# Optimization experiments

Measured on AMD Instinct MI355X. Metric: run time of the kernel, lower is better.

Reference implementation:

```python
import jax, jax.numpy as jnp
import numpy as np

IN_F, T_IN, T_OUT = 8, 96, 32
B = 4096


def _lstm(x, Wih, Whh, b):
    """Standard LSTM (torch gate order i,f,g,o), batch_first. x: [B,T,I] -> [B,T,H].
    Variational dropout with p=0 (eval mode) is identity, so omitted."""
    Bsz = x.shape[0]
    H = Whh.shape[1]
    # precompute input contribution for all timesteps: [B,T,4H]
    xg = jnp.einsum('bti,gi->btg', x, Wih) + b

    def step(carry, xt):
        h, c = carry
        g = xt + h @ Whh.T  # [B,4H]
        i, f, gg, o = jnp.split(g, 4, axis=-1)
        c = jax.nn.sigmoid(f) * c + jax.nn.sigmoid(i) * jnp.tanh(gg)
        h = jax.nn.sigmoid(o) * jnp.tanh(c)
        return (h, c), h

    h0 = jnp.zeros((Bsz, H), x.dtype)
    _, ys = jax.lax.scan(step, (h0, h0), jnp.swapaxes(xg, 0, 1))
    return jnp.swapaxes(ys, 0, 1)


def setup_inputs() -> dict:
    key = jax.random.key(0)
    ks = jax.random.split(key, 16)
    s = 0.1  # init scale
    return {
        'x': jax.random.normal(ks[0], (B, T_IN, IN_F), jnp.float32),
        'e1_Wih': s * jax.random.normal(ks[1], (256, IN_F), jnp.float32),
        'e1_Whh': s * jax.random.normal(ks[2], (256, 64), jnp.float32),
        'e1_b': s * jax.random.normal(ks[3], (256,), jnp.float32),
        'e2_Wih': s * jax.random.normal(ks[4], (4, 64), jnp.float32),
        'e2_Whh': s * jax.random.normal(ks[5], (4, 1), jnp.float32),
        'e2_b': s * jax.random.normal(ks[6], (4,), jnp.float32),
        'd1_Wih': s * jax.random.normal(ks[7], (64, 1), jnp.float32),
        'd1_Whh': s * jax.random.normal(ks[8], (64, 16), jnp.float32),
        'd1_b': s * jax.random.normal(ks[9], (64,), jnp.float32),
        'd2_Wih': s * jax.random.normal(ks[10], (4, 16), jnp.float32),
        'd2_Whh': s * jax.random.normal(ks[11], (4, 1), jnp.float32),
        'd2_b': s * jax.random.normal(ks[12], (4,), jnp.float32),
        'fc1_W': s * jax.random.normal(ks[13], (32, T_IN + T_OUT), jnp.float32),
        'fc1_b': s * jax.random.normal(ks[13], (32,), jnp.float32),
        'fc2_W': s * jax.random.normal(ks[14], (T_OUT, 32), jnp.float32),
        'fc2_b': s * jax.random.normal(ks[15], (T_OUT,), jnp.float32),
    }


def reference(x, e1_Wih, e1_Whh, e1_b, e2_Wih, e2_Whh, e2_b,
              d1_Wih, d1_Whh, d1_b, d2_Wih, d2_Whh, d2_b,
              fc1_W, fc1_b, fc2_W, fc2_b):
    # Encoder: LSTM(in->64) -> LSTM(64->1) -> ReLU
    h = _lstm(x, e1_Wih, e1_Whh, e1_b)
    h = _lstm(h, e2_Wih, e2_Whh, e2_b)
    enc_out = jax.nn.relu(h)  # [B, T_IN, 1]
    # Auxiliary: last T_OUT steps of invocation column (col 0)
    x_aux = x[:, -T_OUT:, 0:1]  # [B, T_OUT, 1]
    dec_in = jnp.concatenate([enc_out, x_aux], axis=1)  # [B, T_IN+T_OUT, 1]
    # Decoder: LSTM(1->16) -> LSTM(16->1)
    d = _lstm(dec_in, d1_Wih, d1_Whh, d1_b)
    d = _lstm(d, d2_Wih, d2_Whh, d2_b)  # [B, T_IN+T_OUT, 1]
    # FC head over the flattened time dim
    flat = d.reshape(-1, T_IN + T_OUT)
    out = flat @ fc1_W.T + fc1_b
    out = out @ fc2_W.T + fc2_b
    return out  # [B, T_OUT]
```

## Files before the change

kernel.cpp:

```cpp
#include <hip/hip_runtime.h>
#include <hip/hip_bf16.h>

typedef __attribute__((ext_vector_type(8))) short bf16x8;
typedef __attribute__((ext_vector_type(4))) float f32x4;

__device__ __forceinline__ float sigm(float x) {
    return __builtin_amdgcn_rcpf(1.0f + __expf(-x));
}
__device__ __forceinline__ float tanh_(float x) {
    float e = __expf(2.0f * x);
    return 1.0f - 2.0f * __builtin_amdgcn_rcpf(e + 1.0f);
}
__device__ __forceinline__ ushort f2bf(float f) {
    uint u = __float_as_uint(f);
    u = u + 0x7FFFu + ((u >> 16) & 1u);
    return (ushort)(u >> 16);
}
__device__ __forceinline__ float bf2f(ushort s) { return __uint_as_float(((uint)s) << 16); }

__global__ __launch_bounds__(1024) __attribute__((amdgpu_waves_per_eu(4, 4)))
void k1_enc(
    const float* __restrict__ x,
    const float* __restrict__ e1_Wih, const float* __restrict__ e1_Whh, const float* __restrict__ e1_b,
    const float* __restrict__ e2_Wih, const float* __restrict__ e2_b,
    const float* __restrict__ e2_Whh,
    float* __restrict__ dec_in)
{
    __shared__ float x_s[16 * 772];
    __shared__ __align__(16) ushort h_hi[2][8][16][8];
    __shared__ __align__(16) ushort h_lo[2][8][16][8];
    __shared__ __align__(16) ushort x2_s[2][4][16][8];
    __shared__ __align__(16) float pe2_s[96 * 64];

    const int t = threadIdx.x;
    const int bBase = blockIdx.x * 16;
    const int wv = t >> 6, l = t & 63;
    const int row = l & 15, sub = l >> 4;

    for (int bb = 0; bb < 16; ++bb)
        for (int i = t; i < 768; i += 1024)
            x_s[bb * 772 + i] = x[(size_t)(bBase + bb) * 768 + i];

    auto loadW = [&](const float* rowbase, int k0, bool valid, bf16x8& hi8, bf16x8& lo8) {
        float f[8];
        if (valid) {
            float4 v0 = ((const float4*)(rowbase + k0))[0];
            float4 v1 = ((const float4*)(rowbase + k0))[1];
            f[0]=v0.x; f[1]=v0.y; f[2]=v0.z; f[3]=v0.w;
            f[4]=v1.x; f[5]=v1.y; f[6]=v1.z; f[7]=v1.w;
        } else {
            #pragma unroll
            for (int j = 0; j < 8; ++j) f[j] = 0.f;
        }
        #pragma unroll
        for (int j = 0; j < 8; ++j) {
            ushort h = f2bf(f[j]);
            hi8[j] = (short)h;
            lo8[j] = (short)f2bf(f[j] - bf2f(h));
        }
    };
    auto loadA = [&](int T, bool isE2, bf16x8& Ah0, bf16x8& Ah1, bf16x8& Al0, bf16x8& Al1, bf16x8& A2) {
        const int gate = row & 3, uq = row >> 2;
        const bool valid = !isE2 || (uq == 0);
        const int wr = isE2 ? gate : gate * 64 + T * 4 + uq;
        const float* rp = isE2 ? (e2_Wih + (size_t)wr * 64) : (e1_Whh + (size_t)wr * 64);
        loadW(rp, sub * 8,      valid, Ah0, Al0);
        loadW(rp, 32 + sub * 8, valid, Ah1, Al1);
        #pragma unroll
        for (int j = 0; j < 8; ++j) A2[j] = 0;
        if (valid) {
            if (!isE2) {
                if (sub < 3) {
                    const float* wihr = e1_Wih + (size_t)wr * 8;
                    #pragma unroll
                    for (int j = 0; j < 8; ++j) {
                        float f = wihr[j];
                        ushort hh = f2bf(f);
                        A2[j] = (sub < 2) ? (short)hh : (short)f2bf(f - bf2f(hh));
                    }
                } else {
                    float bb = e1_b[wr];
                    ushort hh = f2bf(bb);
                    A2[0] = (short)hh; A2[1] = (short)f2bf(bb - bf2f(hh));
                }
            } else if (sub == 3) {
// ... 75 lines not shown
            h_lo[pn][u0_ >> 3][cb][u0_ & 7] = f2bf(hv - bf2f(hh));
        }

        if (ts < 95 && t < 384) {
            int sb = t >> 7, b = (t >> 3) & 15, j = t & 7;
            float xv = x_s[b * 772 + (ts + 1) * 8 + j];
            ushort hi = f2bf(xv);
            x2_s[pn][sb][b][j] = (sb == 1) ? f2bf(xv - bf2f(hi)) : hi;
        }
        __syncthreads();
    }

    if (wv == 15) {
        bf16x8 Bh0 = *(const bf16x8*)&h_hi[0][sub][cb][0];
        bf16x8 Bh1 = *(const bf16x8*)&h_hi[0][4 + sub][cb][0];
        bf16x8 Bl0 = *(const bf16x8*)&h_lo[0][sub][cb][0];
        bf16x8 Bl1 = *(const bf16x8*)&h_lo[0][4 + sub][cb][0];
        bf16x8 Bx  = *(const bf16x8*)&x2_s[0][sub][cb][0];
        f32x4 u2 = {0.f,0.f,0.f,0.f}, v2 = {0.f,0.f,0.f,0.f};
        u2 = __builtin_amdgcn_mfma_f32_16x16x32_bf16(A2h0, Bh0, u2, 0, 0, 0);
        u2 = __builtin_amdgcn_mfma_f32_16x16x32_bf16(A2l0, Bh0, u2, 0, 0, 0);
        u2 = __builtin_amdgcn_mfma_f32_16x16x32_bf16(A2h0, Bl0, u2, 0, 0, 0);
        v2 = __builtin_amdgcn_mfma_f32_16x16x32_bf16(A2h1, Bh1, v2, 0, 0, 0);
        v2 = __builtin_amdgcn_mfma_f32_16x16x32_bf16(A2l1, Bh1, v2, 0, 0, 0);
        v2 = __builtin_amdgcn_mfma_f32_16x16x32_bf16(A2h1, Bl1, v2, 0, 0, 0);
        v2 = __builtin_amdgcn_mfma_f32_16x16x32_bf16(A2x,  Bx,  v2, 0, 0, 0);
        if (sub == 0) {
            f32x4 acc2 = u2 + v2;
            #pragma unroll
            for (int i = 0; i < 4; ++i)
                pe2_s[95 * 64 + i * 16 + cb] = acc2[i];
        }
    }
    __syncthreads();

    if (wv == 0 && l < 16) {
        const float w0 = e2_Whh[0], w1 = e2_Whh[1], w2 = e2_Whh[2], w3 = e2_Whh[3];
        float ni = pe2_s[l], nf = pe2_s[16 + l], ng = pe2_s[32 + l], no = pe2_s[48 + l];
        float h = 0.f, c = 0.f;
        #pragma unroll 1
        for (int ts = 0; ts < 96; ++ts) {
            float gi = ni, gf = nf, gg2 = ng, go = no;
            if (ts < 95) {
                int b2 = (ts + 1) * 64;
                ni = pe2_s[b2 + l]; nf = pe2_s[b2 + 16 + l];
                ng = pe2_s[b2 + 32 + l]; no = pe2_s[b2 + 48 + l];
            }
            gi = fmaf(h, w0, gi);
            gf = fmaf(h, w1, gf);
            gg2 = fmaf(h, w2, gg2);
            go = fmaf(h, w3, go);
            c = fmaf(sigm(gf), c, sigm(gi) * tanh_(gg2));
            h = sigm(go) * tanh_(c);
            dec_in[(size_t)ts * 4096 + bBase + l] = fmaxf(h, 0.f);
        }
    }
    if (wv >= 1 && wv <= 8) {
        int i = (wv - 1) * 64 + l;
        int B = i >> 5, j = i & 31;
        dec_in[(size_t)(96 + j) * 4096 + bBase + B] = x_s[B * 772 + (64 + j) * 8];
    }
}

__global__ __launch_bounds__(256, 2) void k3_dec(
    const float* __restrict__ dec_in,
    const float* __restrict__ d1_Wih, const float* __restrict__ d1_Whh, const float* __restrict__ d1_b,
    const float* __restrict__ d2_Wih, const float* __restrict__ d2_b,
    const float* __restrict__ d2_Whh,
    const float* __restrict__ fc1_W, const float* __restrict__ fc1_b,
    const float* __restrict__ fc2_W, const float* __restrict__ fc2_b,
    float* __restrict__ out)
{
    __shared__ float din_s[16 * 129];
    __shared__ float h_lds[16][16];
    __shared__ float pd2_s[16 * 516];
    __shared__ float d2h_s[16 * 132];
    __shared__ float mid_s[16 * 36];

    const int t = threadIdx.x;
    const int w = t >> 6, lane = t & 63;
    const int qq4 = lane >> 4, u = lane & 15;
    const int row = w * 4 + qq4;
    const size_t bBase = (size_t)blockIdx.x * 16;

    for (int i = t; i < 2048; i += 256) {
        int ts = i >> 4, rr = i & 15;
        din_s[rr * 129 + ts] = dec_in[(size_t)ts * 4096 + bBase + rr];
    }

    float wih_g[4], bg[4], whh_g[4][16], d2w[16];
    #pragma unroll
    for (int g = 0; g < 4; ++g) {
        wih_g[g] = d1_Wih[g * 16 + u];
        bg[g]    = d1_b[g * 16 + u];
        const float4* wp = (const float4*)(d1_Whh + (size_t)(g * 16 + u) * 16);
        #pragma unroll
        for (int k4 = 0; k4 < 4; ++k4) {
            float4 v = wp[k4];
            whh_g[g][4*k4+0] = v.x; whh_g[g][4*k4+1] = v.y;
            whh_g[g][4*k4+2] = v.z; whh_g[g][4*k4+3] = v.w;
        }
    }
    {
        const float4* wp = (const float4*)(d2_Wih + (size_t)(u & 3) * 16);
        #pragma unroll
        for (int k4 = 0; k4 < 4; ++k4) {
            float4 v = wp[k4];
            d2w[4*k4+0] = v.x; d2w[4*k4+1] = v.y; d2w[4*k4+2] = v.z; d2w[4*k4+3] = v.w;
        }
    }
    const float d2bias = d2_b[u & 3];

    float h = 0.f, c = 0.f;
    __syncthreads();

    float hv[16];
    for (int ts = 0; ts < 128; ++ts) {
        float xv = din_s[row * 129 + ts];
        float p0 = fmaf(xv, wih_g[0], bg[0]);
        float p1 = fmaf(xv, wih_g[1], bg[1]);
        float p2 = fmaf(xv, wih_g[2], bg[2]);
        float p3 = fmaf(xv, wih_g[3], bg[3]);
        if (ts > 0) {
            const float4* hp = (const float4*)&h_lds[row][0];
            #pragma unroll
            for (int k4 = 0; k4 < 4; ++k4) {
                float4 v = hp[k4];
                hv[4*k4+0] = v.x; hv[4*k4+1] = v.y; hv[4*k4+2] = v.z; hv[4*k4+3] = v.w;
            }
            #pragma unroll
            for (int k = 0; k < 16; ++k) {
                p0 = fmaf(hv[k], whh_g[0][k], p0);
                p1 = fmaf(hv[k], whh_g[1][k], p1);
                p2 = fmaf(hv[k], whh_g[2][k], p2);
                p3 = fmaf(hv[k], whh_g[3][k], p3);
            }
            if (u < 4) {
                float a = d2bias;
                #pragma unroll
                for (int k = 0; k < 16; ++k) a = fmaf(hv[k], d2w[k], a);
                pd2_s[row * 516 + (ts - 1) * 4 + u] = a;
            }
        }
        c = fmaf(sigm(p1), c, sigm(p0) * tanh_(p2));
        h = sigm(p3) * tanh_(c);
        h_lds[row][u] = h;
    }
    {
        const float4* hp = (const float4*)&h_lds[row][0];
        #pragma unroll
        for (int k4 = 0; k4 < 4; ++k4) {
            float4 v = hp[k4];
            hv[4*k4+0] = v.x; hv[4*k4+1] = v.y; hv[4*k4+2] = v.z; hv[4*k4+3] = v.w;
        }
        if (u < 4) {
            float a = d2bias;
            #pragma unroll
            for (int k = 0; k < 16; ++k) a = fmaf(hv[k], d2w[k], a);
            pd2_s[row * 516 + 127 * 4 + u] = a;
        }
    }
    __syncthreads();

    {
        const float w0 = d2_Whh[0], w1 = d2_Whh[1], w2 = d2_Whh[2], w3 = d2_Whh[3];
        if (t < 16) {
            float4 dbuf[4];
            #pragma unroll
            for (int j = 0; j < 4; ++j) dbuf[j] = *(const float4*)&pd2_s[t * 516 + j * 4];
            float h2 = 0.f, c2 = 0.f;
            #pragma unroll
            for (int ts = 0; ts < 128; ++ts) {
                float4 g4 = dbuf[ts & 3];
                if (ts + 4 < 128) dbuf[ts & 3] = *(const float4*)&pd2_s[t * 516 + (ts + 4) * 4];
                float gi = fmaf(h2, w0, g4.x);
                float gf = fmaf(h2, w1, g4.y);
                float gg = fmaf(h2, w2, g4.z);
                float go = fmaf(h2, w3, g4.w);
                c2 = fmaf(sigm(gf), c2, sigm(gi) * tanh_(gg));
                h2 = sigm(go) * tanh_(c2);
                d2h_s[t * 132 + ts] = h2;
            }
        }
    }
    __syncthreads();

    {
        const int bb = t >> 4, o = t & 15;
        float acc0 = fc1_b[o], acc1 = fc1_b[o + 16];
        const float4* wa = (const float4*)(fc1_W + (size_t)o * 128);
        const float4* wb = (const float4*)(fc1_W + (size_t)(o + 16) * 128);
        const float4* fp = (const float4*)&d2h_s[bb * 132];
        #pragma unroll
        for (int k4 = 0; k4 < 32; ++k4) {
            float4 f = fp[k4], va = wa[k4], vb = wb[k4];
            acc0 = fmaf(f.x, va.x, acc0); acc0 = fmaf(f.y, va.y, acc0);
            acc0 = fmaf(f.z, va.z, acc0); acc0 = fmaf(f.w, va.w, acc0);
            acc1 = fmaf(f.x, vb.x, acc1); acc1 = fmaf(f.y, vb.y, acc1);
            acc1 = fmaf(f.z, vb.z, acc1); acc1 = fmaf(f.w, vb.w, acc1);
        }
        mid_s[bb * 36 + o] = acc0;
        mid_s[bb * 36 + o + 16] = acc1;
        __syncthreads();
        float o0 = fc2_b[o], o1 = fc2_b[o + 16];
        const float4* va2 = (const float4*)(fc2_W + (size_t)o * 32);
        const float4* vb2 = (const float4*)(fc2_W + (size_t)(o + 16) * 32);
        const float4* mp = (const float4*)&mid_s[bb * 36];
        #pragma unroll
        for (int k4 = 0; k4 < 8; ++k4) {
            float4 m = mp[k4], va = va2[k4], vb = vb2[k4];
            o0 = fmaf(m.x, va.x, o0); o0 = fmaf(m.y, va.y, o0);
            o0 = fmaf(m.z, va.z, o0); o0 = fmaf(m.w, va.w, o0);
            o1 = fmaf(m.x, vb.x, o1); o1 = fmaf(m.y, vb.y, o1);
            o1 = fmaf(m.z, vb.z, o1); o1 = fmaf(m.w, vb.w, o1);
        }
        out[(bBase + bb) * 32 + o] = o0;
        out[(bBase + bb) * 32 + o + 16] = o1;
    }
}

extern "C" void kernel_launch(void* const* d_in, const int* in_sizes, int n_in,
                              void* d_out, int out_size, void* d_ws, size_t ws_size,
                              hipStream_t stream) {
    const float* x      = (const float*)d_in[0];
    const float* e1_Wih = (const float*)d_in[1];
    const float* e1_Whh = (const float*)d_in[2];
    const float* e1_b   = (const float*)d_in[3];
    const float* e2_Wih = (const float*)d_in[4];
    const float* e2_Whh = (const float*)d_in[5];
    const float* e2_b   = (const float*)d_in[6];
    const float* d1_Wih = (const float*)d_in[7];
    const float* d1_Whh = (const float*)d_in[8];
    const float* d1_b   = (const float*)d_in[9];
    const float* d2_Wih = (const float*)d_in[10];
    const float* d2_Whh = (const float*)d_in[11];
    const float* d2_b   = (const float*)d_in[12];
    const float* fc1_W  = (const float*)d_in[13];
    const float* fc1_b  = (const float*)d_in[14];
    const float* fc2_W  = (const float*)d_in[15];
    const float* fc2_b  = (const float*)d_in[16];
    float* out = (float*)d_out;

    float* dec_in = (float*)d_ws;

    hipLaunchKernelGGL(k1_enc, dim3(256), dim3(1024), 0, stream,
                       x, e1_Wih, e1_Whh, e1_b, e2_Wih, e2_b, e2_Whh, dec_in);
    hipLaunchKernelGGL(k3_dec, dim3(256), dim3(256), 0, stream,
                       dec_in, d1_Wih, d1_Whh, d1_b, d2_Wih, d2_b, d2_Whh,
                       fc1_W, fc1_b, fc2_W, fc2_b, out);
}
```

Before: 157.3 us.

## Move decoder LSTM recurrence onto bf16 MFMA with split hi/lo precision

```diff
diff --git a/kernel.cpp b/kernel.cpp
--- a/kernel.cpp
+++ b/kernel.cpp
@@ -222,7 +222,8 @@
     }
 }
 
-__global__ __launch_bounds__(256, 2) void k3_dec(
+__global__ __launch_bounds__(512) __attribute__((amdgpu_waves_per_eu(2, 2)))
+void k3_dec(
     const float* __restrict__ dec_in,
     const float* __restrict__ d1_Wih, const float* __restrict__ d1_Whh, const float* __restrict__ d1_b,
     const float* __restrict__ d2_Wih, const float* __restrict__ d2_b,
@@ -231,151 +232,183 @@
     const float* __restrict__ fc2_W, const float* __restrict__ fc2_b,
     float* __restrict__ out)
 {
-    __shared__ float din_s[16 * 129];
-    __shared__ float h_lds[16][16];
-    __shared__ float pd2_s[16 * 516];
-    __shared__ float d2h_s[16 * 132];
-    __shared__ float mid_s[16 * 36];
+    __shared__ float din_s[16][132];
+    __shared__ __align__(16) ushort h_s[8][2][32];
+    __shared__ __align__(16) float pd2_s[8][2][128][4];
+    __shared__ float d2h_s[8][2][128];
+    __shared__ float mid_s[8][2][32];
 
     const int t = threadIdx.x;
-    const int w = t >> 6, lane = t & 63;
-    const int qq4 = lane >> 4, u = lane & 15;
-    const int row = w * 4 + qq4;
+    const int wb = t >> 6, l = t & 63;
+    const int cb = l & 15, sub = l >> 4;
     const size_t bBase = (size_t)blockIdx.x * 16;
 
-    for (int i = t; i < 2048; i += 256) {
-        int ts = i >> 4, rr = i & 15;
-        din_s[rr * 129 + ts] = dec_in[(size_t)ts * 4096 + bBase + rr];
-    }
-
-    float wih_g[4], bg[4], whh_g[4][16], d2w[16];
+    for (int i = t; i < 2048; i += 512) {
+        int ts = i >> 4, bb = i & 15;
+        din_s[bb][ts] = dec_in[(size_t)ts * 4096 + bBase + bb];
+    }
+
+    bf16x8 A1t[5], A2t[5];
+    {
+        const int r = l & 15, g = r & 3, ul = r >> 2;
+        #pragma unroll
+        for (int T = 0; T < 4; ++T) {
+            const int grow = g * 16 + 4 * ul + T;
+            const float* wr = d1_Whh + grow * 16;
+            float wih = d1_Wih[grow], bb = d1_b[grow];
+            ushort wih_hi = f2bf(wih), wih_lo = f2bf(wih - bf2f(wih_hi));
+            ushort b_hi = f2bf(bb),  b_lo  = f2bf(bb - bf2f(b_hi));
+            bf16x8 a1, a2;
+            #pragma unroll
+            for (int j = 0; j < 8; ++j) {
+                int k = sub * 8 + j;
+                float w = wr[k & 15];
+                ushort whi = f2bf(w);
+                a1[j] = (short)whi;
+                if (k < 16) a2[j] = (short)f2bf(w - bf2f(whi));
+                else {
+                    int kk = k - 16;
+                    ushort v = (kk == 0) ? wih_hi : (kk == 1) ? wih_hi :
+                               (kk == 2) ? b_hi   : (kk == 3) ? b_lo   :
+                               (kk == 4) ? wih_lo : (ushort)0;
+                    a2[j] = (short)v;
+                }
+            }
+            A1t[T] = a1; A2t[T] = a2;
+        }
+        {
+            const bool valid = r < 4;
+            const float* wr = d2_Wih + (size_t)(r & 3) * 16;
+            float bb2 = valid ? d2_b[r & 3] : 0.f;
+            ushort b_hi = f2bf(bb2), b_lo = f2bf(bb2 - bf2f(b_hi));
+            bf16x8 a1, a2;
+            #pragma unroll
+            for (int j = 0; j < 8; ++j) {
+                int k = sub * 8 + j;
+                float w = valid ? wr[k & 15] : 0.f;
+                ushort whi = f2bf(w);
+                a1[j] = (short)whi;
+                if (k < 16) a2[j] = (short)f2bf(w - bf2f(whi));
+                else {
+                    int kk = k - 16;
+                    ushort v = (kk == 2) ? b_hi : (kk == 3) ? b_lo : (ushort)0;
+                    a2[j] = valid ? (short)v : (short)0;
+                }
+            }
+            A1t[4] = a1; A2t[4] = a2;
+        }
+    }
+
+    if (l < 64) h_s[wb][l >> 5][l & 31] = 0;
+
+    bf16x8 zero8;
     #pragma unroll
-    for (int g = 0; g < 4; ++g) {
-        wih_g[g] = d1_Wih[g * 16 + u];
-        bg[g]    = d1_b[g * 16 + u];
-        const float4* wp = (const float4*)(d1_Whh + (size_t)(g * 16 + u) * 16);
-        #pragma unroll
-        for (int k4 = 0; k4 < 4; ++k4) {
-            float4 v = wp[k4];
-            whh_g[g][4*k4+0] = v.x; whh_g[g][4*k4+1] = v.y;
-            whh_g[g][4*k4+2] = v.z; whh_g[g][4*k4+3] = v.w;
-        }
-    }
+    for (int j = 0; j < 8; ++j) zero8[j] = 0;
+
+    float c_st[4] = {0.f, 0.f, 0.f, 0.f};
+    const int drow = 2 * wb + (cb & 1);
+    __syncthreads();
+
+    #pragma unroll 1
+    for (int ts = 0; ts < 128; ++ts) {
+        bf16x8 B1 = *(const bf16x8*)&h_s[wb][cb & 1][sub * 8];
+        float xv = din_s[drow][ts];
+        ushort xhi = f2bf(xv), xlo = f2bf(xv - bf2f(xhi));
+        bf16x8 xb = zero8;
+        xb[0] = (short)xhi; xb[1] = (short)xlo;
+        xb[2] = (short)0x3F80; xb[3] = (short)0x3F80; xb[4] = (short)xhi;
+        bf16x8 B2 = (sub < 2) ? B1 : (sub == 2) ? xb : zero8;
+
+        f32x4 z = {0.f, 0.f, 0.f, 0.f};
+        f32x4 a0 = __builtin_amdgcn_mfma_f32_16x16x32_bf16(A1t[0], B1, z, 0, 0, 0);
+        a0 = __builtin_amdgcn_mfma_f32_16x16x32_bf16(A2t[0], B2, a0, 0, 0, 0);
+        f32x4 a1 = __builtin_amdgcn_mfma_f32_16x16x32_bf16(A1t[1], B1, z, 0, 0, 0);
+        a1 = __builtin_amdgcn_mfma_f32_16x16x32_bf16(A2t[1], B2, a1, 0, 0, 0);
+        f32x4 a2 = __builtin_amdgcn_mfma_f32_16x16x32_bf16(A1t[2], B1, z, 0, 0, 0);
+        a2 = __builtin_amdgcn_mfma_f32_16x16x32_bf16(A2t[2], B2, a2, 0, 0, 0);
+        f32x4 a3 = __builtin_amdgcn_mfma_f32_16x16x32_bf16(A1t[3], B1, z, 0, 0, 0);
+        a3 = __builtin_amdgcn_mfma_f32_16x16x32_bf16(A2t[3], B2, a3, 0, 0, 0);
+        f32x4 a4 = __builtin_amdgcn_mfma_f32_16x16x32_bf16(A1t[4], B1, z, 0, 0, 0);
+        a4 = __builtin_amdgcn_mfma_f32_16x16x32_bf16(A2t[4], B2, a4, 0, 0, 0);
+
+        if (ts > 0 && sub == 0 && cb < 2)
+            *(float4*)&pd2_s[wb][cb][ts - 1][0] = make_float4(a4[0], a4[1], a4[2], a4[3]);
+
+        float hn[4];
+        {
+            c_st[0] = fmaf(sigm(a0[1]), c_st[0], sigm(a0[0]) * tanh_(a0[2]));
+            hn[0] = sigm(a0[3]) * tanh_(c_st[0]);
+            c_st[1] = fmaf(sigm(a1[1]), c_st[1], sigm(a1[0]) * tanh_(a1[2]));
+            hn[1] = sigm(a1[3]) * tanh_(c_st[1]);
+            c_st[2] = fmaf(sigm(a2[1]), c_st[2], sigm(a2[0]) * tanh_(a2[2]));
+            hn[2] = sigm(a2[3]) * tanh_(c_st[2]);
+            c_st[3] = fmaf(sigm(a3[1]), c_st[3], sigm(a3[0]) * tanh_(a3[2]));
+            hn[3] = sigm(a3[3]) * tanh_(c_st[3]);
+        }
+        if (cb < 2) {
+            uint2 phi, plo;
+            phi.x = (uint)f2bf(hn[0]) | ((uint)f2bf(hn[1]) << 16);
+            phi.y = (uint)f2bf(hn[2]) | ((uint)f2bf(hn[3]) << 16);
+            plo.x = (uint)f2bf(hn[0] - bf2f(f2bf(hn[0]))) | ((uint)f2bf(hn[1] - bf2f(f2bf(hn[1]))) << 16);
+            plo.y = (uint)f2bf(hn[2] - bf2f(f2bf(hn[2]))) | ((uint)f2bf(hn[3] - bf2f(f2bf(hn[3]))) << 16);
+            *(uint2*)&h_s[wb][cb][4 * sub] = phi;
+            *(uint2*)&h_s[wb][cb][16 + 4 * sub] = plo;
+        }
+    }
+
     {
-        const float4* wp = (const float4*)(d2_Wih + (size_t)(u & 3) * 16);
-        #pragma unroll
-        for (int k4 = 0; k4 < 4; ++k4) {
-            float4 v = wp[k4];
-            d2w[4*k4+0] = v.x; d2w[4*k4+1] = v.y; d2w[4*k4+2] = v.z; d2w[4*k4+3] = v.w;
-        }
-    }
-    const float d2bias = d2_b[u & 3];
-
-    float h = 0.f, c = 0.f;
-    __syncthreads();
-
-    float hv[16];
-    for (int ts = 0; ts < 128; ++ts) {
-        float xv = din_s[row * 129 + ts];
-        float p0 = fmaf(xv, wih_g[0], bg[0]);
-        float p1 = fmaf(xv, wih_g[1], bg[1]);
-        float p2 = fmaf(xv, wih_g[2], bg[2]);
-        float p3 = fmaf(xv, wih_g[3], bg[3]);
-        if (ts > 0) {
-            const float4* hp = (const float4*)&h_lds[row][0];
-            #pragma unroll
-            for (int k4 = 0; k4 < 4; ++k4) {
-                float4 v = hp[k4];
-                hv[4*k4+0] = v.x; hv[4*k4+1] = v.y; hv[4*k4+2] = v.z; hv[4*k4+3] = v.w;
-            }
-            #pragma unroll
-            for (int k = 0; k < 16; ++k) {
-                p0 = fmaf(hv[k], whh_g[0][k], p0);
-                p1 = fmaf(hv[k], whh_g[1][k], p1);
-                p2 = fmaf(hv[k], whh_g[2][k], p2);
-                p3 = fmaf(hv[k], whh_g[3][k], p3);
-            }
-            if (u < 4) {
-                float a = d2bias;
-                #pragma unroll
-                for (int k = 0; k < 16; ++k) a = fmaf(hv[k], d2w[k], a);
-                pd2_s[row * 516 + (ts - 1) * 4 + u] = a;
-            }
-        }
-        c = fmaf(sigm(p1), c, sigm(p0) * tanh_(p2));
-        h = sigm(p3) * tanh_(c);
-        h_lds[row][u] = h;
-    }
+        bf16x8 B1f = *(const bf16x8*)&h_s[wb][cb & 1][sub * 8];
+        bf16x8 onev = zero8; onev[2] = (short)0x3F80; onev[3] = (short)0x3F80;
+        bf16x8 B2f = (sub < 2) ? B1f : (sub == 2) ? onev : zero8;
+        f32x4 z = {0.f, 0.f, 0.f, 0.f};
+        f32x4 a4 = __builtin_amdgcn_mfma_f32_16x16x32_bf16(A1t[4], B1f, z, 0, 0, 0);
+        a4 = __builtin_amdgcn_mfma_f32_16x16x32_bf16(A2t[4], B2f, a4, 0, 0, 0);
+        if (sub == 0 && cb < 2)
+            *(float4*)&pd2_s[wb][cb][127][0] = make_float4(a4[0], a4[1], a4[2], a4[3]);
+    }
+
+    if (l < 2) {
+        const float w0 = d2_Whh[0], w1 = d2_Whh[1], w2 = d2_Whh[2], w3 = d2_Whh[3];
+        float4 dbuf[4];
+        #pragma unroll
+        for (int j = 0; j < 4; ++j) dbuf[j] = *(const float4*)&pd2_s[wb][l][j][0];
+        float h2 = 0.f, c2 = 0.f;
+        #pragma unroll
+        for (int ts = 0; ts < 128; ++ts) {
+            float4 g4 = dbuf[ts & 3];
+            if (ts + 4 < 128) dbuf[ts & 3] = *(const float4*)&pd2_s[wb][l][ts + 4][0];
+            float gi = fmaf(h2, w0, g4.x);
+            float gf = fmaf(h2, w1, g4.y);
+            float gg = fmaf(h2, w2, g4.z);
+            float go = fmaf(h2, w3, g4.w);
+            c2 = fmaf(sigm(gf), c2, sigm(gi) * tanh_(gg));
+            h2 = sigm(go) * tanh_(c2);
+            d2h_s[wb][l][ts] = h2;
+        }
+    }
+
     {
-        const float4* hp = (const float4*)&h_lds[row][0];
-        #pragma unroll
-        for (int k4 = 0; k4 < 4; ++k4) {
-            float4 v = hp[k4];
-            hv[4*k4+0] = v.x; hv[4*k4+1] = v.y; hv[4*k4+2] = v.z; hv[4*k4+3] = v.w;
-        }
-        if (u < 4) {
-            float a = d2bias;
-            #pragma unroll
-            for (int k = 0; k < 16; ++k) a = fmaf(hv[k], d2w[k], a);
-            pd2_s[row * 516 + 127 * 4 + u] = a;
-        }
-    }
-    __syncthreads();
-
-    {
-        const float w0 = d2_Whh[0], w1 = d2_Whh[1], w2 = d2_Whh[2], w3 = d2_Whh[3];
-        if (t < 16) {
-            float4 dbuf[4];
-            #pragma unroll
-            for (int j = 0; j < 4; ++j) dbuf[j] = *(const float4*)&pd2_s[t * 516 + j * 4];
-            float h2 = 0.f, c2 = 0.f;
-            #pragma unroll
-            for (int ts = 0; ts < 128; ++ts) {
-                float4 g4 = dbuf[ts & 3];
-                if (ts + 4 < 128) dbuf[ts & 3] = *(const float4*)&pd2_s[t * 516 + (ts + 4) * 4];
-                float gi = fmaf(h2, w0, g4.x);
-                float gf = fmaf(h2, w1, g4.y);
-                float gg = fmaf(h2, w2, g4.z);
-                float go = fmaf(h2, w3, g4.w);
-                c2 = fmaf(sigm(gf), c2, sigm(gi) * tanh_(gg));
-                h2 = sigm(go) * tanh_(c2);
-                d2h_s[t * 132 + ts] = h2;
-            }
-        }
-    }
-    __syncthreads();
-
-    {
-        const int bb = t >> 4, o = t & 15;
-        float acc0 = fc1_b[o], acc1 = fc1_b[o + 16];
-        const float4* wa = (const float4*)(fc1_W + (size_t)o * 128);
-        const float4* wb = (const float4*)(fc1_W + (size_t)(o + 16) * 128);
-        const float4* fp = (const float4*)&d2h_s[bb * 132];
+        const int cbb = l >> 5, o = l & 31;
+        float acc = fc1_b[o];
+        const float4* wp = (const float4*)(fc1_W + (size_t)o * 128);
+        const float4* fp = (const float4*)&d2h_s[wb][cbb][0];
         #pragma unroll
         for (int k4 = 0; k4 < 32; ++k4) {
-            float4 f = fp[k4], va = wa[k4], vb = wb[k4];
-            acc0 = fmaf(f.x, va.x, acc0); acc0 = fmaf(f.y, va.y, acc0);
-            acc0 = fmaf(f.z, va.z, acc0); acc0 = fmaf(f.w, va.w, acc0);
-            acc1 = fmaf(f.x, vb.x, acc1); acc1 = fmaf(f.y, vb.y, acc1);
-            acc1 = fmaf(f.z, vb.z, acc1); acc1 = fmaf(f.w, vb.w, acc1);
-        }
-        mid_s[bb * 36 + o] = acc0;
-        mid_s[bb * 36 + o + 16] = acc1;
-        __syncthreads();
-        float o0 = fc2_b[o], o1 = fc2_b[o + 16];
-        const float4* va2 = (const float4*)(fc2_W + (size_t)o * 32);
-        const float4* vb2 = (const float4*)(fc2_W + (size_t)(o + 16) * 32);
-        const float4* mp = (const float4*)&mid_s[bb * 36];
+            float4 f = fp[k4], vv = wp[k4];
+            acc = fmaf(f.x, vv.x, acc); acc = fmaf(f.y, vv.y, acc);
+            acc = fmaf(f.z, vv.z, acc); acc = fmaf(f.w, vv.w, acc);
+        }
+        mid_s[wb][cbb][o] = acc;
+        float o2 = fc2_b[o];
+        const float4* w2p = (const float4*)(fc2_W + (size_t)o * 32);
+        const float4* mp = (const float4*)&mid_s[wb][cbb][0];
         #pragma unroll
         for (int k4 = 0; k4 < 8; ++k4) {
-            float4 m = mp[k4], va = va2[k4], vb = vb2[k4];
-            o0 = fmaf(m.x, va.x, o0); o0 = fmaf(m.y, va.y, o0);
-            o0 = fmaf(m.z, va.z, o0); o0 = fmaf(m.w, va.w, o0);
-            o1 = fmaf(m.x, vb.x, o1); o1 = fmaf(m.y, vb.y, o1);
-            o1 = fmaf(m.z, vb.z, o1); o1 = fmaf(m.w, vb.w, o1);
-        }
-        out[(bBase + bb) * 32 + o] = o0;
-        out[(bBase + bb) * 32 + o + 16] = o1;
+            float4 m = mp[k4], vv = w2p[k4];
+            o2 = fmaf(m.x, vv.x, o2); o2 = fmaf(m.y, vv.y, o2);
+            o2 = fmaf(m.z, vv.z, o2); o2 = fmaf(m.w, vv.w, o2);
+        }
+        out[(bBase + 2 * wb + cbb) * 32 + o] = o2;
     }
 }
 
@@ -405,7 +438,7 @@
 
     hipLaunchKernelGGL(k1_enc, dim3(256), dim3(1024), 0, stream,
                        x, e1_Wih, e1_Whh, e1_b, e2_Wih, e2_b, e2_Whh, dec_in);
-    hipLaunchKernelGGL(k3_dec, dim3(256), dim3(256), 0, stream,
+    hipLaunchKernelGGL(k3_dec, dim3(256), dim3(512), 0, stream,
                        dec_in, d1_Wih, d1_Whh, d1_b, d2_Wih, d2_b, d2_Whh,
                        fc1_W, fc1_b, fc2_W, fc2_b, out);
 }
```

New measurement: 240.3 us. 1.53x slower.

## Split decoder LSTM hidden dot across lane pairs and keep each row in one wave

Applied to the files above, without the earlier changes.

```diff
diff --git a/kernel.cpp b/kernel.cpp
--- a/kernel.cpp
+++ b/kernel.cpp
@@ -222,7 +222,8 @@
     }
 }
 
-__global__ __launch_bounds__(256, 2) void k3_dec(
+__global__ __launch_bounds__(512) __attribute__((amdgpu_waves_per_eu(2, 2)))
+void k3_dec(
     const float* __restrict__ dec_in,
     const float* __restrict__ d1_Wih, const float* __restrict__ d1_Whh, const float* __restrict__ d1_b,
     const float* __restrict__ d2_Wih, const float* __restrict__ d2_b,
@@ -231,36 +232,34 @@
     const float* __restrict__ fc2_W, const float* __restrict__ fc2_b,
     float* __restrict__ out)
 {
-    __shared__ float din_s[16 * 129];
-    __shared__ float h_lds[16][16];
-    __shared__ float pd2_s[16 * 516];
-    __shared__ float d2h_s[16 * 132];
-    __shared__ float mid_s[16 * 36];
+    __shared__ float din_s[16][132];
+    __shared__ __align__(16) float h_f[16][20];
+    __shared__ __align__(16) float pd2_s[16][130][4];
+    __shared__ float d2h_s[16][132];
+    __shared__ float mid_s[16][36];
 
     const int t = threadIdx.x;
-    const int w = t >> 6, lane = t & 63;
-    const int qq4 = lane >> 4, u = lane & 15;
-    const int row = w * 4 + qq4;
+    const int w = t >> 6, l = t & 63;
+    const int bp = l >> 5, u = (l >> 1) & 15, kh = l & 1;
+    const int row = 2 * w + bp;
     const size_t bBase = (size_t)blockIdx.x * 16;
 
-    for (int i = t; i < 2048; i += 256) {
-        int ts = i >> 4, rr = i & 15;
-        din_s[rr * 129 + ts] = dec_in[(size_t)ts * 4096 + bBase + rr];
-    }
-
-    float wih_g[4], bg[4], whh_g[4][16], d2w[16];
+    for (int i = t; i < 2048; i += 512) {
+        int ts = i >> 4, bb = i & 15;
+        din_s[bb][ts] = dec_in[(size_t)ts * 4096 + bBase + bb];
+    }
+
+    float whh_h[4][8], wih_g[4], bg4[4];
     #pragma unroll
     for (int g = 0; g < 4; ++g) {
+        const float4* wp = (const float4*)(d1_Whh + (size_t)(g * 16 + u) * 16 + kh * 8);
+        float4 v0 = wp[0], v1 = wp[1];
+        whh_h[g][0]=v0.x; whh_h[g][1]=v0.y; whh_h[g][2]=v0.z; whh_h[g][3]=v0.w;
+        whh_h[g][4]=v1.x; whh_h[g][5]=v1.y; whh_h[g][6]=v1.z; whh_h[g][7]=v1.w;
         wih_g[g] = d1_Wih[g * 16 + u];
-        bg[g]    = d1_b[g * 16 + u];
-        const float4* wp = (const float4*)(d1_Whh + (size_t)(g * 16 + u) * 16);
-        #pragma unroll
-        for (int k4 = 0; k4 < 4; ++k4) {
-            float4 v = wp[k4];
-            whh_g[g][4*k4+0] = v.x; whh_g[g][4*k4+1] = v.y;
-            whh_g[g][4*k4+2] = v.z; whh_g[g][4*k4+3] = v.w;
-        }
-    }
+        bg4[g]   = d1_b[g * 16 + u];
+    }
+    float d2w[16];
     {
         const float4* wp = (const float4*)(d2_Wih + (size_t)(u & 3) * 16);
         #pragma unroll
@@ -271,111 +270,102 @@
     }
     const float d2bias = d2_b[u & 3];
 
-    float h = 0.f, c = 0.f;
+    float c_u = 0.f;
+    if (kh == 0) h_f[row][u] = 0.f;
     __syncthreads();
 
-    float hv[16];
+    #pragma unroll 1
     for (int ts = 0; ts < 128; ++ts) {
-        float xv = din_s[row * 129 + ts];
-        float p0 = fmaf(xv, wih_g[0], bg[0]);
-        float p1 = fmaf(xv, wih_g[1], bg[1]);
-        float p2 = fmaf(xv, wih_g[2], bg[2]);
-        float p3 = fmaf(xv, wih_g[3], bg[3]);
+        float xv = din_s[row][ts];
+        float p0, p1, p2, p3;
+        if (kh == 0) {
+            p0 = fmaf(xv, wih_g[0], bg4[0]);
+            p1 = fmaf(xv, wih_g[1], bg4[1]);
+            p2 = fmaf(xv, wih_g[2], bg4[2]);
+            p3 = fmaf(xv, wih_g[3], bg4[3]);
+        } else {
+            p0 = p1 = p2 = p3 = 0.f;
+        }
         if (ts > 0) {
-            const float4* hp = (const float4*)&h_lds[row][0];
+            const float4* hp = (const float4*)&h_f[row][kh * 8];
+            float4 a = hp[0], b = hp[1];
+            float hv[8] = {a.x, a.y, a.z, a.w, b.x, b.y, b.z, b.w};
             #pragma unroll
-            for (int k4 = 0; k4 < 4; ++k4) {
-                float4 v = hp[k4];
-                hv[4*k4+0] = v.x; hv[4*k4+1] = v.y; hv[4*k4+2] = v.z; hv[4*k4+3] = v.w;
+            for (int k = 0; k < 8; ++k) {
+                p0 = fmaf(hv[k], whh_h[0][k], p0);
+                p1 = fmaf(hv[k], whh_h[1][k], p1);
+                p2 = fmaf(hv[k], whh_h[2][k], p2);
+                p3 = fmaf(hv[k], whh_h[3][k], p3);
             }
-            #pragma unroll
-            for (int k = 0; k < 16; ++k) {
-                p0 = fmaf(hv[k], whh_g[0][k], p0);
-                p1 = fmaf(hv[k], whh_g[1][k], p1);
-                p2 = fmaf(hv[k], whh_g[2][k], p2);
-                p3 = fmaf(hv[k], whh_g[3][k], p3);
-            }
-            if (u < 4) {
-                float a = d2bias;
-                #pragma unroll
-                for (int k = 0; k < 16; ++k) a = fmaf(hv[k], d2w[k], a);
-                pd2_s[row * 516 + (ts - 1) * 4 + u] = a;
-            }
-        }
-        c = fmaf(sigm(p1), c, sigm(p0) * tanh_(p2));
-        h = sigm(p3) * tanh_(c);
-        h_lds[row][u] = h;
-    }
+        }
+        p0 += __shfl_xor(p0, 1);
+        p1 += __shfl_xor(p1, 1);
+        p2 += __shfl_xor(p2, 1);
+        p3 += __shfl_xor(p3, 1);
+
+        if (kh == 0) {
+            c_u = fmaf(sigm(p1), c_u, sigm(p0) * tanh_(p2));
+            float hnew = sigm(p3) * tanh_(c_u);
+            h_f[row][u] = hnew;
+        }
+        if (kh == 0 && u < 4) {
+            const float4* hp2 = (const float4*)&h_f[row][0];
+            float4 h0 = hp2[0], h1 = hp2[1], h2 = hp2[2], h3 = hp2[3];
+            float a = d2bias;
+            a = fmaf(h0.x, d2w[0],  a); a = fmaf(h0.y, d2w[1],  a);
+            a = fmaf(h0.z, d2w[2],  a); a = fmaf(h0.w, d2w[3],  a);
+            a = fmaf(h1.x, d2w[4],  a); a = fmaf(h1.y, d2w[5],  a);
+            a = fmaf(h1.z, d2w[6],  a); a = fmaf(h1.w, d2w[7],  a);
+            a = fmaf(h2.x, d2w[8],  a); a = fmaf(h2.y, d2w[9],  a);
+            a = fmaf(h2.z, d2w[10], a); a = fmaf(h2.w, d2w[11], a);
+            a = fmaf(h3.x, d2w[12], a); a = fmaf(h3.y, d2w[13], a);
+            a = fmaf(h3.z, d2w[14], a); a = fmaf(h3.w, d2w[15], a);
+            pd2_s[row][ts][u] = a;
+        }
+    }
+
+    if ((l & 31) == 0) {
+        const float w0 = d2_Whh[0], w1 = d2_Whh[1], w2 = d2_Whh[2], w3 = d2_Whh[3];
+        float4 dbuf[4];
+        #pragma unroll
+        for (int j = 0; j < 4; ++j) dbuf[j] = *(const float4*)&pd2_s[row][j][0];
+        float h2 = 0.f, c2 = 0.f;
+        #pragma unroll
+        for (int ts = 0; ts < 128; ++ts) {
+            float4 g4 = dbuf[ts & 3];
+            if (ts + 4 < 128) dbuf[ts & 3] = *(const float4*)&pd2_s[row][ts + 4][0];
+            float gi = fmaf(h2, w0, g4.x);
+            float gf = fmaf(h2, w1, g4.y);
+            float gg = fmaf(h2, w2, g4.z);
+            float go = fmaf(h2, w3, g4.w);
+            c2 = fmaf(sigm(gf), c2, sigm(gi) * tanh_(gg));
+            h2 = sigm(go) * tanh_(c2);
+            d2h_s[row][ts] = h2;
+        }
+    }
+
     {
-        const float4* hp = (const float4*)&h_lds[row][0];
-        #pragma unroll
-        for (int k4 = 0; k4 < 4; ++k4) {
-            float4 v = hp[k4];
-            hv[4*k4+0] = v.x; hv[4*k4+1] = v.y; hv[4*k4+2] = v.z; hv[4*k4+3] = v.w;
-        }
-        if (u < 4) {
-            float a = d2bias;
-            #pragma unroll
-            for (int k = 0; k < 16; ++k) a = fmaf(hv[k], d2w[k], a);
-            pd2_s[row * 516 + 127 * 4 + u] = a;
-        }
-    }
-    __syncthreads();
-
-    {
-        const float w0 = d2_Whh[0], w1 = d2_Whh[1], w2 = d2_Whh[2], w3 = d2_Whh[3];
-        if (t < 16) {
-            float4 dbuf[4];
-            #pragma unroll
-            for (int j = 0; j < 4; ++j) dbuf[j] = *(const float4*)&pd2_s[t * 516 + j * 4];
-            float h2 = 0.f, c2 = 0.f;
-            #pragma unroll
-            for (int ts = 0; ts < 128; ++ts) {
-                float4 g4 = dbuf[ts & 3];
-                if (ts + 4 < 128) dbuf[ts & 3] = *(const float4*)&pd2_s[t * 516 + (ts + 4) * 4];
-                float gi = fmaf(h2, w0, g4.x);
-                float gf = fmaf(h2, w1, g4.y);
-                float gg = fmaf(h2, w2, g4.z);
-                float go = fmaf(h2, w3, g4.w);
-                c2 = fmaf(sigm(gf), c2, sigm(gi) * tanh_(gg));
-                h2 = sigm(go) * tanh_(c2);
-                d2h_s[t * 132 + ts] = h2;
-            }
-        }
-    }
-    __syncthreads();
-
-    {
-        const int bb = t >> 4, o = t & 15;
-        float acc0 = fc1_b[o], acc1 = fc1_b[o + 16];
-        const float4* wa = (const float4*)(fc1_W + (size_t)o * 128);
-        const float4* wb = (const float4*)(fc1_W + (size_t)(o + 16) * 128);
-        const float4* fp = (const float4*)&d2h_s[bb * 132];
+        const int o = l & 31, rowf = 2 * w + (l >> 5);
+        float acc = fc1_b[o];
+        const float4* wp = (const float4*)(fc1_W + (size_t)o * 128);
+        const float4* fp = (const float4*)&d2h_s[rowf][0];
         #pragma unroll
         for (int k4 = 0; k4 < 32; ++k4) {
-            float4 f = fp[k4], va = wa[k4], vb = wb[k4];
-            acc0 = fmaf(f.x, va.x, acc0); acc0 = fmaf(f.y, va.y, acc0);
-            acc0 = fmaf(f.z, va.z, acc0); acc0 = fmaf(f.w, va.w, acc0);
-            acc1 = fmaf(f.x, vb.x, acc1); acc1 = fmaf(f.y, vb.y, acc1);
-            acc1 = fmaf(f.z, vb.z, acc1); acc1 = fmaf(f.w, vb.w, acc1);
-        }
-        mid_s[bb * 36 + o] = acc0;
-        mid_s[bb * 36 + o + 16] = acc1;
-        __syncthreads();
-        float o0 = fc2_b[o], o1 = fc2_b[o + 16];
-        const float4* va2 = (const float4*)(fc2_W + (size_t)o * 32);
-        const float4* vb2 = (const float4*)(fc2_W + (size_t)(o + 16) * 32);
-        const float4* mp = (const float4*)&mid_s[bb * 36];
+            float4 f = fp[k4], vv = wp[k4];
+            acc = fmaf(f.x, vv.x, acc); acc = fmaf(f.y, vv.y, acc);
+            acc = fmaf(f.z, vv.z, acc); acc = fmaf(f.w, vv.w, acc);
+        }
+        mid_s[rowf][o] = acc;
+        float o2 = fc2_b[o];
+        const float4* w2p = (const float4*)(fc2_W + (size_t)o * 32);
+        const float4* mp = (const float4*)&mid_s[rowf][0];
         #pragma unroll
         for (int k4 = 0; k4 < 8; ++k4) {
-            float4 m = mp[k4], va = va2[k4], vb = vb2[k4];
-            o0 = fmaf(m.x, va.x, o0); o0 = fmaf(m.y, va.y, o0);
-            o0 = fmaf(m.z, va.z, o0); o0 = fmaf(m.w, va.w, o0);
-            o1 = fmaf(m.x, vb.x, o1); o1 = fmaf(m.y, vb.y, o1);
-            o1 = fmaf(m.z, vb.z, o1); o1 = fmaf(m.w, vb.w, o1);
-        }
-        out[(bBase + bb) * 32 + o] = o0;
-        out[(bBase + bb) * 32 + o + 16] = o1;
+            float4 m = mp[k4], vv = w2p[k4];
+            o2 = fmaf(m.x, vv.x, o2); o2 = fmaf(m.y, vv.y, o2);
+            o2 = fmaf(m.z, vv.z, o2); o2 = fmaf(m.w, vv.w, o2);
+        }
+        out[(bBase + rowf) * 32 + o] = o2;
     }
 }
 
@@ -405,7 +395,7 @@
 
     hipLaunchKernelGGL(k1_enc, dim3(256), dim3(1024), 0, stream,
                        x, e1_Wih, e1_Whh, e1_b, e2_Wih, e2_b, e2_Whh, dec_in);
-    hipLaunchKernelGGL(k3_dec, dim3(256), dim3(256), 0, stream,
+    hipLaunchKernelGGL(k3_dec, dim3(256), dim3(512), 0, stream,
                        dec_in, d1_Wih, d1_Whh, d1_b, d2_Wih, d2_b, d2_Whh,
                        fc1_W, fc1_b, fc2_W, fc2_b, out);
 }
```

Measured after the change: 180.5 us. +14.8%, slower.

## Fuse encoder and decoder kernels into one block-resident kernel

Applied to the files above, without the earlier changes.

```diff
diff --git a/kernel.cpp b/kernel.cpp
--- a/kernel.cpp
+++ b/kernel.cpp
@@ -19,18 +19,28 @@
 __device__ __forceinline__ float bf2f(ushort s) { return __uint_as_float(((uint)s) << 16); }
 
 __global__ __launch_bounds__(1024) __attribute__((amdgpu_waves_per_eu(4, 4)))
-void k1_enc(
+void fused_all(
     const float* __restrict__ x,
     const float* __restrict__ e1_Wih, const float* __restrict__ e1_Whh, const float* __restrict__ e1_b,
     const float* __restrict__ e2_Wih, const float* __restrict__ e2_b,
     const float* __restrict__ e2_Whh,
-    float* __restrict__ dec_in)
+    const float* __restrict__ d1_Wih, const float* __restrict__ d1_Whh, const float* __restrict__ d1_b,
+    const float* __restrict__ d2_Wih, const float* __restrict__ d2_b,
+    const float* __restrict__ d2_Whh,
+    const float* __restrict__ fc1_W, const float* __restrict__ fc1_b,
+    const float* __restrict__ fc2_W, const float* __restrict__ fc2_b,
+    float* __restrict__ out)
 {
     __shared__ float x_s[16 * 772];
     __shared__ __align__(16) ushort h_hi[2][8][16][8];
     __shared__ __align__(16) ushort h_lo[2][8][16][8];
     __shared__ __align__(16) ushort x2_s[2][4][16][8];
     __shared__ __align__(16) float pe2_s[96 * 64];
+    __shared__ float din_s[16][132];
+    __shared__ float h_lds[16][16];
+    __shared__ float pd2_s[16 * 516];
+    __shared__ float d2h_s[16 * 132];
+    __shared__ float mid_s[16 * 36];
 
     const int t = threadIdx.x;
     const int bBase = blockIdx.x * 16;
@@ -212,119 +222,98 @@
             go = fmaf(h, w3, go);
             c = fmaf(sigm(gf), c, sigm(gi) * tanh_(gg2));
             h = sigm(go) * tanh_(c);
-            dec_in[(size_t)ts * 4096 + bBase + l] = fmaxf(h, 0.f);
+            din_s[l][ts] = fmaxf(h, 0.f);
         }
     }
     if (wv >= 1 && wv <= 8) {
         int i = (wv - 1) * 64 + l;
         int B = i >> 5, j = i & 31;
-        dec_in[(size_t)(96 + j) * 4096 + bBase + B] = x_s[B * 772 + (64 + j) * 8];
-    }
-}
-
-__global__ __launch_bounds__(256, 2) void k3_dec(
-    const float* __restrict__ dec_in,
-    const float* __restrict__ d1_Wih, const float* __restrict__ d1_Whh, const float* __restrict__ d1_b,
-    const float* __restrict__ d2_Wih, const float* __restrict__ d2_b,
-    const float* __restrict__ d2_Whh,
-    const float* __restrict__ fc1_W, const float* __restrict__ fc1_b,
-    const float* __restrict__ fc2_W, const float* __restrict__ fc2_b,
-    float* __restrict__ out)
-{
-    __shared__ float din_s[16 * 129];
-    __shared__ float h_lds[16][16];
-    __shared__ float pd2_s[16 * 516];
-    __shared__ float d2h_s[16 * 132];
-    __shared__ float mid_s[16 * 36];
-
-    const int t = threadIdx.x;
-    const int w = t >> 6, lane = t & 63;
-    const int qq4 = lane >> 4, u = lane & 15;
-    const int row = w * 4 + qq4;
-    const size_t bBase = (size_t)blockIdx.x * 16;
-
-    for (int i = t; i < 2048; i += 256) {
-        int ts = i >> 4, rr = i & 15;
-        din_s[rr * 129 + ts] = dec_in[(size_t)ts * 4096 + bBase + rr];
-    }
-
-    float wih_g[4], bg[4], whh_g[4][16], d2w[16];
-    #pragma unroll
-    for (int g = 0; g < 4; ++g) {
-        wih_g[g] = d1_Wih[g * 16 + u];
-        bg[g]    = d1_b[g * 16 + u];
-        const float4* wp = (const float4*)(d1_Whh + (size_t)(g * 16 + u) * 16);
-        #pragma unroll
-        for (int k4 = 0; k4 < 4; ++k4) {
-            float4 v = wp[k4];
-            whh_g[g][4*k4+0] = v.x; whh_g[g][4*k4+1] = v.y;
-            whh_g[g][4*k4+2] = v.z; whh_g[g][4*k4+3] = v.w;
-        }
-    }
+        din_s[B][96 + j] = x_s[B * 772 + (64 + j) * 8];
+    }
+    __syncthreads();
+
     {
-        const float4* wp = (const float4*)(d2_Wih + (size_t)(u & 3) * 16);
-        #pragma unroll
-        for (int k4 = 0; k4 < 4; ++k4) {
-            float4 v = wp[k4];
-            d2w[4*k4+0] = v.x; d2w[4*k4+1] = v.y; d2w[4*k4+2] = v.z; d2w[4*k4+3] = v.w;
-        }
-    }
-    const float d2bias = d2_b[u & 3];
-
-    float h = 0.f, c = 0.f;
-    __syncthreads();
-
-    float hv[16];
-    for (int ts = 0; ts < 128; ++ts) {
-        float xv = din_s[row * 129 + ts];
-        float p0 = fmaf(xv, wih_g[0], bg[0]);
-        float p1 = fmaf(xv, wih_g[1], bg[1]);
-        float p2 = fmaf(xv, wih_g[2], bg[2]);
-        float p3 = fmaf(xv, wih_g[3], bg[3]);
-        if (ts > 0) {
-            const float4* hp = (const float4*)&h_lds[row][0];
-            #pragma unroll
-            for (int k4 = 0; k4 < 4; ++k4) {
-                float4 v = hp[k4];
-                hv[4*k4+0] = v.x; hv[4*k4+1] = v.y; hv[4*k4+2] = v.z; hv[4*k4+3] = v.w;
-            }
-            #pragma unroll
-            for (int k = 0; k < 16; ++k) {
-                p0 = fmaf(hv[k], whh_g[0][k], p0);
-                p1 = fmaf(hv[k], whh_g[1][k], p1);
-                p2 = fmaf(hv[k], whh_g[2][k], p2);
-                p3 = fmaf(hv[k], whh_g[3][k], p3);
-            }
-            if (u < 4) {
-                float a = d2bias;
+        const int dw = t >> 6, dlane = t & 63;
+        const int dq = dlane >> 4, du = dlane & 15;
+        const int drow = dw * 4 + dq;
+
+        if (t < 256) {
+            float wih_g[4], bg[4], whh_g[4][16], d2w[16];
+            #pragma unroll
+            for (int g = 0; g < 4; ++g) {
+                wih_g[g] = d1_Wih[g * 16 + du];
+                bg[g]    = d1_b[g * 16 + du];
+                const float4* wp = (const float4*)(d1_Whh + (size_t)(g * 16 + du) * 16);
                 #pragma unroll
-                for (int k = 0; k < 16; ++k) a = fmaf(hv[k], d2w[k], a);
-                pd2_s[row * 516 + (ts - 1) * 4 + u] = a;
-            }
-        }
-        c = fmaf(sigm(p1), c, sigm(p0) * tanh_(p2));
-        h = sigm(p3) * tanh_(c);
-        h_lds[row][u] = h;
-    }
-    {
-        const float4* hp = (const float4*)&h_lds[row][0];
-        #pragma unroll
-        for (int k4 = 0; k4 < 4; ++k4) {
-            float4 v = hp[k4];
-            hv[4*k4+0] = v.x; hv[4*k4+1] = v.y; hv[4*k4+2] = v.z; hv[4*k4+3] = v.w;
-        }
-        if (u < 4) {
-            float a = d2bias;
-            #pragma unroll
-            for (int k = 0; k < 16; ++k) a = fmaf(hv[k], d2w[k], a);
-            pd2_s[row * 516 + 127 * 4 + u] = a;
-        }
-    }
-    __syncthreads();
-
-    {
-        const float w0 = d2_Whh[0], w1 = d2_Whh[1], w2 = d2_Whh[2], w3 = d2_Whh[3];
+                for (int k4 = 0; k4 < 4; ++k4) {
+                    float4 v = wp[k4];
+                    whh_g[g][4*k4+0] = v.x; whh_g[g][4*k4+1] = v.y;
+                    whh_g[g][4*k4+2] = v.z; whh_g[g][4*k4+3] = v.w;
+                }
+            }
+            {
+                const float4* wp = (const float4*)(d2_Wih + (size_t)(du & 3) * 16);
+                #pragma unroll
+                for (int k4 = 0; k4 < 4; ++k4) {
+                    float4 v = wp[k4];
+                    d2w[4*k4+0] = v.x; d2w[4*k4+1] = v.y; d2w[4*k4+2] = v.z; d2w[4*k4+3] = v.w;
+                }
+            }
+            const float d2bias = d2_b[du & 3];
+
+            float h = 0.f, c = 0.f;
+            float hv[16];
+            #pragma unroll 1
+            for (int ts = 0; ts < 128; ++ts) {
+                float xv = din_s[drow][ts];
+                float p0 = fmaf(xv, wih_g[0], bg[0]);
+                float p1 = fmaf(xv, wih_g[1], bg[1]);
+                float p2 = fmaf(xv, wih_g[2], bg[2]);
+                float p3 = fmaf(xv, wih_g[3], bg[3]);
+                if (ts > 0) {
+                    const float4* hp = (const float4*)&h_lds[drow][0];
+                    #pragma unroll
+                    for (int k4 = 0; k4 < 4; ++k4) {
+                        float4 v = hp[k4];
+                        hv[4*k4+0] = v.x; hv[4*k4+1] = v.y; hv[4*k4+2] = v.z; hv[4*k4+3] = v.w;
+                    }
+                    #pragma unroll
+                    for (int k = 0; k < 16; ++k) {
+                        p0 = fmaf(hv[k], whh_g[0][k], p0);
+                        p1 = fmaf(hv[k], whh_g[1][k], p1);
+                        p2 = fmaf(hv[k], whh_g[2][k], p2);
+                        p3 = fmaf(hv[k], whh_g[3][k], p3);
+                    }
+                    if (du < 4) {
+                        float a = d2bias;
+                        #pragma unroll
+                        for (int k = 0; k < 16; ++k) a = fmaf(hv[k], d2w[k], a);
+                        pd2_s[drow * 516 + (ts - 1) * 4 + du] = a;
+                    }
+                }
+                c = fmaf(sigm(p1), c, sigm(p0) * tanh_(p2));
+                h = sigm(p3) * tanh_(c);
+                h_lds[drow][du] = h;
+            }
+            {
+                const float4* hp = (const float4*)&h_lds[drow][0];
+                #pragma unroll
+                for (int k4 = 0; k4 < 4; ++k4) {
+                    float4 v = hp[k4];
+                    hv[4*k4+0] = v.x; hv[4*k4+1] = v.y; hv[4*k4+2] = v.z; hv[4*k4+3] = v.w;
+                }
+                if (du < 4) {
+                    float a = d2bias;
+                    #pragma unroll
+                    for (int k = 0; k < 16; ++k) a = fmaf(hv[k], d2w[k], a);
+                    pd2_s[drow * 516 + 127 * 4 + du] = a;
+                }
+            }
+        }
+        __syncthreads();
+
         if (t < 16) {
+            const float w0 = d2_Whh[0], w1 = d2_Whh[1], w2 = d2_Whh[2], w3 = d2_Whh[3];
             float4 dbuf[4];
             #pragma unroll
             for (int j = 0; j < 4; ++j) dbuf[j] = *(const float4*)&pd2_s[t * 516 + j * 4];
@@ -342,40 +331,44 @@
                 d2h_s[t * 132 + ts] = h2;
             }
         }
-    }
-    __syncthreads();
-
-    {
-        const int bb = t >> 4, o = t & 15;
-        float acc0 = fc1_b[o], acc1 = fc1_b[o + 16];
-        const float4* wa = (const float4*)(fc1_W + (size_t)o * 128);
-        const float4* wb = (const float4*)(fc1_W + (size_t)(o + 16) * 128);
-        const float4* fp = (const float4*)&d2h_s[bb * 132];
-        #pragma unroll
-        for (int k4 = 0; k4 < 32; ++k4) {
-            float4 f = fp[k4], va = wa[k4], vb = wb[k4];
-            acc0 = fmaf(f.x, va.x, acc0); acc0 = fmaf(f.y, va.y, acc0);
-            acc0 = fmaf(f.z, va.z, acc0); acc0 = fmaf(f.w, va.w, acc0);
-            acc1 = fmaf(f.x, vb.x, acc1); acc1 = fmaf(f.y, vb.y, acc1);
-            acc1 = fmaf(f.z, vb.z, acc1); acc1 = fmaf(f.w, vb.w, acc1);
-        }
-        mid_s[bb * 36 + o] = acc0;
-        mid_s[bb * 36 + o + 16] = acc1;
         __syncthreads();
-        float o0 = fc2_b[o], o1 = fc2_b[o + 16];
-        const float4* va2 = (const float4*)(fc2_W + (size_t)o * 32);
-        const float4* vb2 = (const float4*)(fc2_W + (size_t)(o + 16) * 32);
-        const float4* mp = (const float4*)&mid_s[bb * 36];
-        #pragma unroll
-        for (int k4 = 0; k4 < 8; ++k4) {
-            float4 m = mp[k4], va = va2[k4], vb = vb2[k4];
-            o0 = fmaf(m.x, va.x, o0); o0 = fmaf(m.y, va.y, o0);
-            o0 = fmaf(m.z, va.z, o0); o0 = fmaf(m.w, va.w, o0);
-            o1 = fmaf(m.x, vb.x, o1); o1 = fmaf(m.y, vb.y, o1);
-            o1 = fmaf(m.z, vb.z, o1); o1 = fmaf(m.w, vb.w, o1);
-        }
-        out[(bBase + bb) * 32 + o] = o0;
-        out[(bBase + bb) * 32 + o + 16] = o1;
+
+        if (t < 256) {
+            const int bb = t >> 4, o = t & 15;
+            float acc0 = fc1_b[o], acc1 = fc1_b[o + 16];
+            const float4* wa = (const float4*)(fc1_W + (size_t)o * 128);
+            const float4* wb = (const float4*)(fc1_W + (size_t)(o + 16) * 128);
+            const float4* fp = (const float4*)&d2h_s[bb * 132];
+            #pragma unroll
+            for (int k4 = 0; k4 < 32; ++k4) {
+                float4 f = fp[k4], va = wa[k4], vb = wb[k4];
+                acc0 = fmaf(f.x, va.x, acc0); acc0 = fmaf(f.y, va.y, acc0);
+                acc0 = fmaf(f.z, va.z, acc0); acc0 = fmaf(f.w, va.w, acc0);
+                acc1 = fmaf(f.x, vb.x, acc1); acc1 = fmaf(f.y, vb.y, acc1);
+                acc1 = fmaf(f.z, vb.z, acc1); acc1 = fmaf(f.w, vb.w, acc1);
+            }
+            mid_s[bb * 36 + o] = acc0;
+            mid_s[bb * 36 + o + 16] = acc1;
+        }
+        __syncthreads();
+
+        if (t < 256) {
+            const int bb = t >> 4, o = t & 15;
+            float o0 = fc2_b[o], o1 = fc2_b[o + 16];
+            const float4* va2 = (const float4*)(fc2_W + (size_t)o * 32);
+            const float4* vb2 = (const float4*)(fc2_W + (size_t)(o + 16) * 32);
+            const float4* mp = (const float4*)&mid_s[bb * 36];
+            #pragma unroll
+            for (int k4 = 0; k4 < 8; ++k4) {
+                float4 m = mp[k4], va = va2[k4], vb = vb2[k4];
+                o0 = fmaf(m.x, va.x, o0); o0 = fmaf(m.y, va.y, o0);
+                o0 = fmaf(m.z, va.z, o0); o0 = fmaf(m.w, va.w, o0);
+                o1 = fmaf(m.x, vb.x, o1); o1 = fmaf(m.y, vb.y, o1);
+                o1 = fmaf(m.z, vb.z, o1); o1 = fmaf(m.w, vb.w, o1);
+            }
+            out[((size_t)bBase + bb) * 32 + o] = o0;
+            out[((size_t)bBase + bb) * 32 + o + 16] = o1;
+        }
     }
 }
 
@@ -401,11 +394,8 @@
     const float* fc2_b  = (const float*)d_in[16];
     float* out = (float*)d_out;
 
-    float* dec_in = (float*)d_ws;
-
-    hipLaunchKernelGGL(k1_enc, dim3(256), dim3(1024), 0, stream,
-                       x, e1_Wih, e1_Whh, e1_b, e2_Wih, e2_b, e2_Whh, dec_in);
-    hipLaunchKernelGGL(k3_dec, dim3(256), dim3(256), 0, stream,
-                       dec_in, d1_Wih, d1_Whh, d1_b, d2_Wih, d2_b, d2_Whh,
+    hipLaunchKernelGGL(fused_all, dim3(256), dim3(1024), 0, stream,
+                       x, e1_Wih, e1_Whh, e1_b, e2_Wih, e2_b, e2_Whh,
+                       d1_Wih, d1_Whh, d1_b, d2_Wih, d2_b, d2_Whh,
                        fc1_W, fc1_b, fc2_W, fc2_b, out);
 }
```

Result: faster. 149.7 us (median of 3 runs) (-4.8%).
